# Kernel optimization log

Hardware: AMD Instinct MI355X
Metric: run time of the kernel (lower is better)

Reference implementation:

```python
import jax, jax.numpy as jnp
import numpy as np

EMB = 256
HID = 256
VOCAB = 32000
NUM_CELLS = 2
BATCH = 64
SEQ = 512


def setup_inputs() -> dict:
    key = jax.random.key(0)
    ks = jax.random.split(key, 6)
    scale = 1.0 / np.sqrt(HID)
    inp = {
        "input": jax.random.randint(ks[0], (BATCH, SEQ), 0, VOCAB, dtype=jnp.int32),
        # explicit routing table: token id -> LSTMCell index
        "assignment": (jnp.arange(VOCAB, dtype=jnp.int32) % NUM_CELLS),
        "embeddings": jax.random.normal(ks[1], (VOCAB, EMB), jnp.float32) * 0.02,
        # stacked per-cell LSTMCell params, torch gate order (i, f, g, o)
        "W_ih": jax.random.uniform(ks[2], (NUM_CELLS, 4 * HID, EMB), jnp.float32, -scale, scale),
        "W_hh": jax.random.uniform(ks[3], (NUM_CELLS, 4 * HID, HID), jnp.float32, -scale, scale),
        "b_ih": jax.random.uniform(ks[4], (NUM_CELLS, 4 * HID), jnp.float32, -scale, scale),
        "b_hh": jax.random.uniform(ks[5], (NUM_CELLS, 4 * HID), jnp.float32, -scale, scale),
    }
    return inp


def reference(input, assignment, embeddings, W_ih, W_hh, b_ih, b_hh):
    B, S = input.shape
    H = W_hh.shape[-1]
    x = embeddings[input]            # [B, S, E]
    a = assignment[input]            # [B, S] cell index per token
    bias = (b_ih + b_hh)[:, None, :]  # [C, 1, 4H]

    def step(carry, ts):
        h, c = carry                 # [B, H] each
        x_t, a_t = ts                # [B, E], [B]
        # gates for every cell, then per-token select (routed dispatch)
        gates = (jnp.einsum('be,cge->cbg', x_t, W_ih)
                 + jnp.einsum('bh,cgh->cbg', h, W_hh)
                 + bias)             # [C, B, 4H]
        g = jnp.take_along_axis(gates, a_t[None, :, None], axis=0)[0]  # [B, 4H]
        i_g, f_g, g_g, o_g = jnp.split(g, 4, axis=-1)
        c_new = jax.nn.sigmoid(f_g) * c + jax.nn.sigmoid(i_g) * jnp.tanh(g_g)
        h_new = jax.nn.sigmoid(o_g) * jnp.tanh(c_new)
        return (h_new, c_new), None

    h0 = jnp.zeros((B, H), x.dtype)
    (h, c), _ = jax.lax.scan(step, (h0, h0),
                             (jnp.swapaxes(x, 0, 1), jnp.swapaxes(a, 0, 1)))
    return jnp.concatenate([h, c], axis=-1)  # [B, 2H]
```

## Files before the change

### kernel.cpp

```cpp
#include <hip/hip_runtime.h>
#include <stdint.h>
#include <stddef.h>


#define BB   64
#define SS   512
#define EE   256
#define HH   256
#define G4   1024
#define NWG  64
#define TPB  512
#define TCH  16

typedef __attribute__((ext_vector_type(8))) short short8;
typedef __attribute__((ext_vector_type(4))) float f32x4;
typedef __attribute__((ext_vector_type(4))) unsigned int uint4v;

__device__ __forceinline__ unsigned short f2bf(float f){
  union { float f; unsigned u; } v; v.f = f;
  return (unsigned short)((v.u + 0x7fffu + ((v.u >> 16) & 1u)) >> 16);
}
__device__ __forceinline__ float bf2f(unsigned short s){
  union { float f; unsigned u; } v; v.u = ((unsigned)s) << 16;
  return v.f;
}
__device__ __forceinline__ int swz3(int byte){ return byte ^ (((byte >> 7) & 3) << 4); }

#define WS_H_OFF  1024
#define WS_XG_OFF (1024 + 131072)

__global__ void zero_ws_kernel(int* ws){
  const int n = (WS_H_OFF + 131072) / 4;
  for (int i = blockIdx.x * blockDim.x + threadIdx.x; i < n; i += gridDim.x * blockDim.x){
    int* p = ws + i;
    const int z = 0;
    asm volatile("global_store_dword %0, %1, off sc0 sc1" :: "v"(p), "v"(z) : "memory");
  }
}

__global__ __launch_bounds__(TPB, 1)
void xproj_kernel(const int* __restrict__ input, const int* __restrict__ assign,
                  const float* __restrict__ emb, const float* __restrict__ Wih,
                  const float* __restrict__ bih, const float* __restrict__ bhh,
                  float* __restrict__ xg)
{
  __shared__ __align__(16) unsigned short sXp[8][4][4][16][8];
  __shared__ int sTokP[TCH][64];
  __shared__ int sAsgP[TCH][64];

  const int tid  = threadIdx.x;
  const int lane = tid & 63;
  const int lg   = lane >> 4;
  const int lc   = lane & 15;
  const int wv   = tid >> 6;
  const int rowtile = blockIdx.x & 15;
  const int tc      = blockIdx.x >> 4;

  const int rbase = rowtile * 128 + wv * 16;
  const int cellw = rbase >> 10;
  const int rrw   = rbase & 1023;

  short8 aX[8];
  {
    const float* pw = Wih + ((size_t)cellw * G4 + (rrw + lc)) * EE + lg * 8;
    #pragma unroll
    for (int kc = 0; kc < 8; ++kc){
      const f32x4 u = *(const f32x4*)(pw + kc * 32);
      const f32x4 v = *(const f32x4*)(pw + kc * 32 + 4);
      short8 x8;
      #pragma unroll
      for (int e = 0; e < 4; ++e){ x8[e] = (short)f2bf(u[e]); x8[4+e] = (short)f2bf(v[e]); }
      aX[kc] = x8;
    }
  }
  float biasr[4];
  #pragma unroll
  for (int q = 0; q < 4; ++q){
    const int idx = cellw * G4 + rrw + lg * 4 + q;
    biasr[q] = bih[idx] + bhh[idx];
  }

  for (int i = tid; i < TCH * 64; i += TPB){
    const int tl = i >> 6, b = i & 63;
    const int tok = input[b * SS + tc * TCH + tl];
    sTokP[tl][b] = tok; sAsgP[tl][b] = assign[tok];
  }
  __syncthreads();

  const int gkc = tid >> 6, glg = (tid >> 4) & 3, glc = tid & 15;
  short8 xr[4];
  auto GATHERP = [&](int tl){
    #pragma unroll
    for (int ct = 0; ct < 4; ++ct){
      const int tok = sTokP[tl][ct * 16 + glc];
      const float* ep = emb + (size_t)tok * EE + gkc * 32 + glg * 8;
      const f32x4 u = *(const f32x4*)ep;
      const f32x4 v = *(const f32x4*)(ep + 4);
      short8 x8;
      #pragma unroll
      for (int e = 0; e < 4; ++e){ x8[e] = (short)f2bf(u[e]); x8[4+e] = (short)f2bf(v[e]); }
      xr[ct] = x8;
    }
  };
  GATHERP(0);

  for (int tl = 0; tl < TCH; ++tl){
    #pragma unroll
    for (int ct = 0; ct < 4; ++ct)
      *(short8*)&sXp[gkc][glg][ct][glc][0] = xr[ct];
    __syncthreads();
    if (tl + 1 < TCH) GATHERP(tl + 1);

    f32x4 acc[4];
    #pragma unroll
    for (int ct = 0; ct < 4; ++ct){
      acc[ct][0] = biasr[0]; acc[ct][1] = biasr[1];
      acc[ct][2] = biasr[2]; acc[ct][3] = biasr[3];
    }
    #pragma unroll
    for (int kc = 0; kc < 8; ++kc){
      #pragma unroll
      for (int ct = 0; ct < 4; ++ct){
        const short8 bx = *(const short8*)&sXp[kc][lg][ct][lc][0];
        acc[ct] = __builtin_amdgcn_mfma_f32_16x16x32_bf16(aX[kc], bx, acc[ct], 0, 0, 0);
      }
    }
    float* xgt = xg + (size_t)(tc * TCH + tl) * 65536;
    #pragma unroll
    for (int ct = 0; ct < 4; ++ct){
      const int b = ct * 16 + lc;
      if (sAsgP[tl][b] == cellw){
        #pragma unroll
        for (int q = 0; q < 4; ++q)
          xgt[(rrw + lg * 4 + q) * 64 + b] = acc[ct][q];
      }
    }
    __syncthreads();
  }
}

__global__ __launch_bounds__(TPB, 1)
void mlstm_rec_kernel(const int* __restrict__ input, const int* __restrict__ assign,
                      const float* __restrict__ Whh, float* __restrict__ out,
                      char* __restrict__ ws)
{
  __shared__ __align__(16) unsigned short sH[4096];
  __shared__ float sC[16][17];
  __shared__ int sAsg[3][64];

  const int tid  = threadIdx.x;
  const int lane = tid & 63;
  const int lg   = lane >> 4;
  const int lc   = lane & 15;
  const int wv   = tid >> 6;
  const int cell = wv & 1;
  const int jq   = wv >> 1;
  const int wg   = blockIdx.x;
  const int jset = wg & 15;
  const int pool = wg >> 4;

  unsigned int* hbuf = (unsigned int*)(ws + WS_H_OFF);
  const float* xg = (const float*)(ws + WS_XG_OFF);

  short8 aHiH[8], aLoH[8];
  {
    const float* ph = Whh + ((size_t)cell * G4 + (lc & 3) * HH
                             + jset * 16 + jq * 4 + (lc >> 2)) * HH + lg * 8;
    #pragma unroll
    for (int kc = 0; kc < 8; ++kc){
      const f32x4 u = *(const f32x4*)(ph + kc * 32);
      const f32x4 v = *(const f32x4*)(ph + kc * 32 + 4);
      short8 hi, lo;
      #pragma unroll
      for (int e = 0; e < 4; ++e){
        const float w0 = u[e], w1 = v[e];
        const unsigned short h0 = f2bf(w0), h1 = f2bf(w1);
        hi[e] = (short)h0;   lo[e] = (short)f2bf(w0 - bf2f(h0));
        hi[4+e] = (short)h1; lo[4+e] = (short)f2bf(w1 - bf2f(h1));
      }
      aHiH[kc] = hi; aLoH[kc] = lo;
    }
  }

  if (tid < 64){
    const int t0 = input[tid * SS];     sAsg[0][tid] = assign[t0];
    const int t1 = input[tid * SS + 1]; sAsg[1][tid] = assign[t1];
  }

  const int jloc   = jq * 4 + lg;
  const int jglob  = jset * 16 + jloc;
  const int b_loc  = lc;
  const int b_glob = pool * 16 + lc;

  float xpre[4];
  auto XPRE = [&](int t){
    const float* p = xg + (size_t)t * 65536 + jglob * 64 + b_glob;
    #pragma unroll
    for (int q = 0; q < 4; ++q)
      xpre[q] = p[q * 16384];
  };
  XPRE(0);
  __syncthreads();

  for (int t = 0; t < SS; ++t){
    f32x4 acc;
    #pragma unroll
    for (int q = 0; q < 4; ++q) acc[q] = xpre[q];
    if (t + 1 < SS) XPRE(t + 1);
    if (t + 2 < SS && tid < 64){
      const int tk = input[tid * SS + (t + 2)];
      sAsg[(t + 2) % 3][tid] = assign[tk];
    }

    if (t > 0){
      const unsigned int* bw = hbuf + (size_t)(t & 1) * 16384 + pool * 4096;
      const unsigned int need = (unsigned int)t;

      uint4v h0, h1;
      unsigned bad;
      const unsigned int* p0 = bw + tid * 8;
      do {
        asm volatile("global_load_dwordx4 %0, %1, off sc0 sc1" : "=v"(h0) : "v"(p0)     : "memory");
        asm volatile("global_load_dwordx4 %0, %1, off sc0 sc1" : "=v"(h1) : "v"(p0 + 4) : "memory");
        asm volatile("s_waitcnt vmcnt(0)" ::: "memory");
        bad = 0;
        #pragma unroll
        for (int e = 0; e < 4; ++e){ bad |= (h0[e] ^ need); bad |= (h1[e] ^ need); }
        bad &= 0xFFFFu;
        if (bad) __builtin_amdgcn_s_sleep(1);
      } while (bad);
      __builtin_amdgcn_sched_barrier(0);

      uint4v pk;
      pk[0] = (h0[0] >> 16) | (h0[1] & 0xFFFF0000u);
      pk[1] = (h0[2] >> 16) | (h0[3] & 0xFFFF0000u);
      pk[2] = (h1[0] >> 16) | (h1[1] & 0xFFFF0000u);
      pk[3] = (h1[2] >> 16) | (h1[3] & 0xFFFF0000u);
      *(uint4v*)((char*)sH + swz3(tid * 16)) = pk;
      __syncthreads();
    }

    if (t > 0){
      #pragma unroll
      for (int kch = 0; kch < 8; ++kch){
        const int js = kch * 2 + (lg >> 1);
        const int byte = js * 512 + lc * 32 + (lg & 1) * 16;
        const short8 hh = *(const short8*)((const char*)sH + swz3(byte));
        acc = __builtin_amdgcn_mfma_f32_16x16x32_bf16(aHiH[kch], hh, acc, 0, 0, 0);
        acc = __builtin_amdgcn_mfma_f32_16x16x32_bf16(aLoH[kch], hh, acc, 0, 0, 0);
      }
    }

    {
      const int a = sAsg[t % 3][b_glob];
      if (a == cell){
        const float gi = acc[0], gf = acc[1], gg = acc[2], go = acc[3];
        const float cold = (t == 0) ? 0.f : sC[b_loc][jloc];
        const float si = 1.f / (1.f + __expf(-gi));
        const float sf = 1.f / (1.f + __expf(-gf));
        const float so = 1.f / (1.f + __expf(-go));
        const float cn = sf * cold + si * tanhf(gg);
        const float hn = so * tanhf(cn);
        if (t < SS - 1){
          sC[b_loc][jloc] = cn;
          const unsigned word = ((unsigned)f2bf(hn) << 16) | ((unsigned)(t + 1) & 0xFFFFu);
          unsigned int* dst = hbuf + (size_t)((t & 1) ^ 1) * 16384 + pool * 4096
                            + jset * 256 + b_loc * 16 + jloc;
          asm volatile("global_store_dword %0, %1, off sc0 sc1" :: "v"(dst), "v"(word) : "memory");
        } else {
          out[b_glob * 512 + jglob]       = hn;
          out[b_glob * 512 + 256 + jglob] = cn;
        }
      }
    }
  }
}

extern "C" void kernel_launch(void* const* d_in, const int* in_sizes, int n_in,
                              void* d_out, int out_size, void* d_ws, size_t ws_size,
                              hipStream_t stream)
{
  const int*   input  = (const int*)  d_in[0];
  const int*   assign = (const int*)  d_in[1];
  const float* emb    = (const float*)d_in[2];
  const float* Wih    = (const float*)d_in[3];
  const float* Whh    = (const float*)d_in[4];
  const float* bih    = (const float*)d_in[5];
  const float* bhh    = (const float*)d_in[6];
  float* out = (float*)d_out;
  char*  ws  = (char*)d_ws;

  zero_ws_kernel<<<64, 256, 0, stream>>>((int*)ws);
  float* xg = (float*)(ws + WS_XG_OFF);
  xproj_kernel<<<512, TPB, 0, stream>>>(input, assign, emb, Wih, bih, bhh, xg);
  mlstm_rec_kernel<<<NWG, TPB, 0, stream>>>(input, assign, Whh, out, ws);
}
```

Baseline: 1.112 ms.

## Fuse input projection and recurrence into one kernel with per-chunk ready flags

Merges the input-projection kernel and the recurrent kernel into a single launch. 64 blocks run the recurrence while the other 192 blocks produce projected gate chunks. Each projection block publishes a done flag per chunk, and the recurrent blocks poll those flags before reading the next 16 timesteps. This lets the projection overlap the sequential recurrence instead of running before it. The risks are that spin-waiting can stall the recurrence if projection blocks fall behind, and that correctness relies on all 256 blocks being co-resident, which the LDS padding is meant to help with.

```diff
diff --git a/kernel.cpp b/kernel.cpp
--- a/kernel.cpp
+++ b/kernel.cpp
@@ -8,7 +8,8 @@
 #define EE   256
 #define HH   256
 #define G4   1024
-#define NWG  64
+#define NREC 64
+#define NB   256
 #define TPB  512
 #define TCH  16
 
@@ -39,128 +40,138 @@
 }
 
 __global__ __launch_bounds__(TPB, 1)
-void xproj_kernel(const int* __restrict__ input, const int* __restrict__ assign,
-                  const float* __restrict__ emb, const float* __restrict__ Wih,
-                  const float* __restrict__ bih, const float* __restrict__ bhh,
-                  float* __restrict__ xg)
+void mlstm_fused_kernel(const int* __restrict__ input, const int* __restrict__ assign,
+                        const float* __restrict__ emb, const float* __restrict__ Wih,
+                        const float* __restrict__ Whh, const float* __restrict__ bih,
+                        const float* __restrict__ bhh, float* __restrict__ out,
+                        char* __restrict__ ws)
 {
   __shared__ __align__(16) unsigned short sXp[8][4][4][16][8];
   __shared__ int sTokP[TCH][64];
   __shared__ int sAsgP[TCH][64];
+  __shared__ __align__(16) unsigned short sH[4096];
+  __shared__ float sC[16][17];
+  __shared__ int sAsg[3][64];
+  __shared__ char sPad[40960];
 
   const int tid  = threadIdx.x;
   const int lane = tid & 63;
   const int lg   = lane >> 4;
   const int lc   = lane & 15;
   const int wv   = tid >> 6;
-  const int rowtile = blockIdx.x & 15;
-  const int tc      = blockIdx.x >> 4;
-
-  const int rbase = rowtile * 128 + wv * 16;
-  const int cellw = rbase >> 10;
-  const int rrw   = rbase & 1023;
-
-  short8 aX[8];
-  {
-    const float* pw = Wih + ((size_t)cellw * G4 + (rrw + lc)) * EE + lg * 8;
-    #pragma unroll
-    for (int kc = 0; kc < 8; ++kc){
-      const f32x4 u = *(const f32x4*)(pw + kc * 32);
-      const f32x4 v = *(const f32x4*)(pw + kc * 32 + 4);
-      short8 x8;
+
+  unsigned short* done = (unsigned short*)ws;
+  unsigned int* hbuf = (unsigned int*)(ws + WS_H_OFF);
+  float* xg = (float*)(ws + WS_XG_OFF);
+
+  if (tid == 1) ((volatile char*)sPad)[0] = 0;
+
+  if (blockIdx.x >= NREC){
+    for (int tau = blockIdx.x - NREC; tau < 512; tau += (NB - NREC)){
+      const int tc      = tau >> 4;
+      const int rowtile = tau & 15;
+
+      const int rbase = rowtile * 128 + wv * 16;
+      const int cellw = rbase >> 10;
+      const int rrw   = rbase & 1023;
+
+      short8 aX[8];
+      {
+        const float* pw = Wih + ((size_t)cellw * G4 + (rrw + lc)) * EE + lg * 8;
+        #pragma unroll
+        for (int kc = 0; kc < 8; ++kc){
+          const f32x4 u = *(const f32x4*)(pw + kc * 32);
+          const f32x4 v = *(const f32x4*)(pw + kc * 32 + 4);
+          short8 x8;
+          #pragma unroll
+          for (int e = 0; e < 4; ++e){ x8[e] = (short)f2bf(u[e]); x8[4+e] = (short)f2bf(v[e]); }
+          aX[kc] = x8;
+        }
+      }
+      float biasr[4];
       #pragma unroll
-      for (int e = 0; e < 4; ++e){ x8[e] = (short)f2bf(u[e]); x8[4+e] = (short)f2bf(v[e]); }
-      aX[kc] = x8;
-    }
-  }
-  float biasr[4];
-  #pragma unroll
-  for (int q = 0; q < 4; ++q){
-    const int idx = cellw * G4 + rrw + lg * 4 + q;
-    biasr[q] = bih[idx] + bhh[idx];
-  }
-
-  for (int i = tid; i < TCH * 64; i += TPB){
-    const int tl = i >> 6, b = i & 63;
-    const int tok = input[b * SS + tc * TCH + tl];
-    sTokP[tl][b] = tok; sAsgP[tl][b] = assign[tok];
-  }
-  __syncthreads();
-
-  const int gkc = tid >> 6, glg = (tid >> 4) & 3, glc = tid & 15;
-  short8 xr[4];
-  auto GATHERP = [&](int tl){
-    #pragma unroll
-    for (int ct = 0; ct < 4; ++ct){
-      const int tok = sTokP[tl][ct * 16 + glc];
-      const float* ep = emb + (size_t)tok * EE + gkc * 32 + glg * 8;
-      const f32x4 u = *(const f32x4*)ep;
-      const f32x4 v = *(const f32x4*)(ep + 4);
-      short8 x8;
-      #pragma unroll
-      for (int e = 0; e < 4; ++e){ x8[e] = (short)f2bf(u[e]); x8[4+e] = (short)f2bf(v[e]); }
-      xr[ct] = x8;
-    }
-  };
-  GATHERP(0);
-
-  for (int tl = 0; tl < TCH; ++tl){
-    #pragma unroll
-    for (int ct = 0; ct < 4; ++ct)
-      *(short8*)&sXp[gkc][glg][ct][glc][0] = xr[ct];
-    __syncthreads();
-    if (tl + 1 < TCH) GATHERP(tl + 1);
-
-    f32x4 acc[4];
-    #pragma unroll
-    for (int ct = 0; ct < 4; ++ct){
-      acc[ct][0] = biasr[0]; acc[ct][1] = biasr[1];
-      acc[ct][2] = biasr[2]; acc[ct][3] = biasr[3];
-    }
-    #pragma unroll
-    for (int kc = 0; kc < 8; ++kc){
-      #pragma unroll
-      for (int ct = 0; ct < 4; ++ct){
-        const short8 bx = *(const short8*)&sXp[kc][lg][ct][lc][0];
-        acc[ct] = __builtin_amdgcn_mfma_f32_16x16x32_bf16(aX[kc], bx, acc[ct], 0, 0, 0);
-      }
-    }
-    float* xgt = xg + (size_t)(tc * TCH + tl) * 65536;
-    #pragma unroll
-    for (int ct = 0; ct < 4; ++ct){
-      const int b = ct * 16 + lc;
-      if (sAsgP[tl][b] == cellw){
-        #pragma unroll
-        for (int q = 0; q < 4; ++q)
-          xgt[(rrw + lg * 4 + q) * 64 + b] = acc[ct][q];
-      }
-    }
-    __syncthreads();
-  }
-}
-
-__global__ __launch_bounds__(TPB, 1)
-void mlstm_rec_kernel(const int* __restrict__ input, const int* __restrict__ assign,
-                      const float* __restrict__ Whh, float* __restrict__ out,
-                      char* __restrict__ ws)
-{
-  __shared__ __align__(16) unsigned short sH[4096];
-  __shared__ float sC[16][17];
-  __shared__ int sAsg[3][64];
-
-  const int tid  = threadIdx.x;
-  const int lane = tid & 63;
-  const int lg   = lane >> 4;
-  const int lc   = lane & 15;
-  const int wv   = tid >> 6;
+      for (int q = 0; q < 4; ++q){
+        const int idx = cellw * G4 + rrw + lg * 4 + q;
+        biasr[q] = bih[idx] + bhh[idx];
+      }
+
+      for (int i = tid; i < TCH * 64; i += TPB){
+        const int tl = i >> 6, b = i & 63;
+        const int tok = input[b * SS + tc * TCH + tl];
+        sTokP[tl][b] = tok; sAsgP[tl][b] = assign[tok];
+      }
+      __syncthreads();
+
+      const int gkc = tid >> 6, glg = (tid >> 4) & 3, glc = tid & 15;
+      short8 xr[4];
+      auto GATHERP = [&](int tl){
+        #pragma unroll
+        for (int ct = 0; ct < 4; ++ct){
+          const int tok = sTokP[tl][ct * 16 + glc];
+          const float* ep = emb + (size_t)tok * EE + gkc * 32 + glg * 8;
+          const f32x4 u = *(const f32x4*)ep;
+          const f32x4 v = *(const f32x4*)(ep + 4);
+          short8 x8;
+          #pragma unroll
+          for (int e = 0; e < 4; ++e){ x8[e] = (short)f2bf(u[e]); x8[4+e] = (short)f2bf(v[e]); }
+          xr[ct] = x8;
+        }
+      };
+      GATHERP(0);
+
+      for (int tl = 0; tl < TCH; ++tl){
+        #pragma unroll
+        for (int ct = 0; ct < 4; ++ct)
+          *(short8*)&sXp[gkc][glg][ct][glc][0] = xr[ct];
+        __syncthreads();
+        if (tl + 1 < TCH) GATHERP(tl + 1);
+
+        f32x4 acc[4];
+        #pragma unroll
+        for (int ct = 0; ct < 4; ++ct){
+          acc[ct][0] = biasr[0]; acc[ct][1] = biasr[1];
+          acc[ct][2] = biasr[2]; acc[ct][3] = biasr[3];
+        }
+        #pragma unroll
+        for (int kc = 0; kc < 8; ++kc){
+          #pragma unroll
+          for (int ct = 0; ct < 4; ++ct){
+            const short8 bx = *(const short8*)&sXp[kc][lg][ct][lc][0];
+            acc[ct] = __builtin_amdgcn_mfma_f32_16x16x32_bf16(aX[kc], bx, acc[ct], 0, 0, 0);
+          }
+        }
+        float* xgt = xg + (size_t)(tc * TCH + tl) * 65536;
+        #pragma unroll
+        for (int ct = 0; ct < 4; ++ct){
+          const int b = ct * 16 + lc;
+          if (sAsgP[tl][b] == cellw){
+            #pragma unroll
+            for (int q = 0; q < 4; ++q){
+              float* dst = xgt + (rrw + lg * 4 + q) * 64 + b;
+              const float val = acc[ct][q];
+              asm volatile("global_store_dword %0, %1, off sc0 sc1" :: "v"(dst), "v"(val) : "memory");
+            }
+          }
+        }
+        __syncthreads();
+      }
+
+      asm volatile("s_waitcnt vmcnt(0)" ::: "memory");
+      __syncthreads();
+      if (tid == 0){
+        unsigned short* fp = done + tau;
+        const unsigned one = 1;
+        asm volatile("global_store_short %0, %1, off sc0 sc1" :: "v"(fp), "v"(one) : "memory");
+      }
+    }
+    return;
+  }
+
   const int cell = wv & 1;
   const int jq   = wv >> 1;
   const int wg   = blockIdx.x;
   const int jset = wg & 15;
   const int pool = wg >> 4;
-
-  unsigned int* hbuf = (unsigned int*)(ws + WS_H_OFF);
-  const float* xg = (const float*)(ws + WS_XG_OFF);
 
   short8 aHiH[8], aLoH[8];
   {
@@ -199,6 +210,19 @@
     for (int q = 0; q < 4; ++q)
       xpre[q] = p[q * 16384];
   };
+  auto WAITCHUNK = [&](int c){
+    const unsigned short* dp = done + c * 16 + (lane & 15);
+    int ok;
+    do {
+      unsigned v;
+      asm volatile("global_load_ushort %0, %1, off sc0 sc1\n\ts_waitcnt vmcnt(0)"
+                   : "=v"(v) : "v"(dp) : "memory");
+      ok = (__ballot(v != 1u) == 0ull);
+      if (!ok) __builtin_amdgcn_s_sleep(8);
+    } while (!ok);
+  };
+
+  WAITCHUNK(0);
   XPRE(0);
   __syncthreads();
 
@@ -206,7 +230,10 @@
     f32x4 acc;
     #pragma unroll
     for (int q = 0; q < 4; ++q) acc[q] = xpre[q];
-    if (t + 1 < SS) XPRE(t + 1);
+    if (t + 1 < SS){
+      if (((t + 1) & 15) == 0) WAITCHUNK((t + 1) >> 4);
+      XPRE(t + 1);
+    }
     if (t + 2 < SS && tid < 64){
       const int tk = input[tid * SS + (t + 2)];
       sAsg[(t + 2) % 3][tid] = assign[tk];
@@ -291,7 +318,6 @@
   char*  ws  = (char*)d_ws;
 
   zero_ws_kernel<<<64, 256, 0, stream>>>((int*)ws);
-  float* xg = (float*)(ws + WS_XG_OFF);
-  xproj_kernel<<<512, TPB, 0, stream>>>(input, assign, emb, Wih, bih, bhh, xg);
-  mlstm_rec_kernel<<<NWG, TPB, 0, stream>>>(input, assign, Whh, out, ws);
-}
+  mlstm_fused_kernel<<<NB, TPB, 0, stream>>>(input, assign, emb, Wih, Whh,
+                                             bih, bhh, out, ws);
+}
```

Result: no change. 1.093 ms (-1.8%).
